# Kernel tuning notes

Hardware: AMD Instinct MI355X
Metric: run time of the kernel (lower is better)

## Reference

```python
import jax, jax.numpy as jnp
import numpy as np

MARGIN = 0.1
LAMBDA_EFFECT = 0.5

B, T_V, K, T_S = 32, 8192, 64, 128


def setup_inputs() -> dict:
    key = jax.random.key(0)
    k1, k2, k3, k4, k5 = jax.random.split(key, 5)
    pred_orig = jax.random.normal(k1, (B, T_V), dtype=jnp.float32)
    pred_intervened = jax.random.normal(k2, (K, B, T_V), dtype=jnp.float32)
    intervened_indices = jax.random.randint(k3, (K,), 0, T_S, dtype=jnp.int32)
    # GT alignment mask: sparse-ish binary alignment between frames and sentences
    gt_mask = jax.random.bernoulli(k4, 0.2, (B, T_V, T_S)).astype(jnp.int32)
    # prefix-valid video mask: valid length per batch in [T_V//2, T_V]
    lengths = jax.random.randint(k5, (B,), T_V // 2, T_V + 1, dtype=jnp.int32)
    mask_video = (jnp.arange(T_V, dtype=jnp.int32)[None, :] < lengths[:, None]).astype(jnp.int32)
    return {
        "pred_orig": pred_orig,
        "pred_intervened": pred_intervened,
        "intervened_indices": intervened_indices,
        "gt_mask": gt_mask,
        "mask_video": mask_video,
    }


def reference(pred_orig, pred_intervened, intervened_indices, gt_mask, mask_video):
    # pred_orig: [B,T], pred_intervened: [K,B,T], gt_mask: [B,T,S], mask_video: [B,T]
    prob_orig = jax.nn.sigmoid(pred_orig)                 # [B,T]
    prob_int = jax.nn.sigmoid(pred_intervened)            # [K,B,T]
    effect = jnp.abs(prob_orig[None, :, :] - prob_int)    # [K,B,T]

    valid = mask_video.astype(bool)                       # [B,T] (prefix mask == :T_v_valid slice)
    # gather intervened sentence columns: [B,T,K] -> [K,B,T]
    gt_sel = jnp.transpose(gt_mask[:, :, intervened_indices], (2, 0, 1))

    aligned = (gt_sel > 0) & valid[None]                  # [K,B,T]
    non_aligned = (gt_sel == 0) & valid[None]             # [K,B,T]

    cnt_a = aligned.sum(axis=-1)                          # [K,B]
    cnt_n = non_aligned.sum(axis=-1)                      # [K,B]

    ea = jnp.sum(effect * aligned, axis=-1) / jnp.maximum(cnt_a, 1)
    en = jnp.sum(effect * non_aligned, axis=-1) / jnp.maximum(cnt_n, 1)

    per_pair = jnp.where((cnt_a > 0) & (cnt_n > 0),
                         jax.nn.relu(MARGIN - (ea - en)),
                         jnp.zeros_like(ea))
    num_interventions = pred_orig.shape[0] * pred_intervened.shape[0]
    alignment_consistency = per_pair.sum() / max(num_interventions, 1)
    total_intervention_loss = alignment_consistency * LAMBDA_EFFECT
    return alignment_consistency, total_intervention_loss
```

## Files before the change

### kernel.cpp

```cpp
#include <hip/hip_runtime.h>
#include <cstdint>

#define BB 32
#define TV 8192
#define KK 64
#define TS 128
#define MARGIN_F 0.1f
#define LAMBDA_F 0.5f

#define TT 256
static constexpr int KSTR = BB * TV;
static constexpr int NTILE = TV / TT;


__global__ __launch_bounds__(256, 4) void fused_kernel(
    const float* __restrict__ po, const float* __restrict__ pi,
    const int* __restrict__ idx, const int* __restrict__ gt,
    const int* __restrict__ mv,
    float* __restrict__ gsa, float* __restrict__ gsv,
    float* __restrict__ gca, int* __restrict__ len) {
  const int tid = threadIdx.x;
  const int lane = tid & 63;
  const int w = tid >> 6;
  const int tile = blockIdx.x & (NTILE - 1);
  const int b = blockIdx.x >> 5;
  const int t0 = tile * TT;

  __shared__ unsigned long long planes[4][65];
  __shared__ unsigned long long sVg[4];
  __shared__ float so[TT];
  __shared__ float saL[KK][65];
  __shared__ float svL[KK][65];

  const int r0 = b * TV + t0 + w * 64;
  const unsigned long long V = __ballot(mv[r0 + lane] != 0);
  if (lane == 0) {
    sVg[w] = V;
    if (V) atomicAdd(&len[b], __popcll(V));
  }
  so[tid] = __fdividef(1.f, 1.f + __expf(-po[b * TV + t0 + tid]));

  const int c = idx[lane];
  const int csel = c & 3, csh = c >> 2;
  unsigned long long plane = 0ull;
  if (V != 0ull) {
    const int4* rowp = (const int4*)(gt + (size_t)r0 * TS);
#pragma unroll 4
    for (int ch = 0; ch < 32; ++ch) {
      int4 v = rowp[ch * 64 + lane];
      unsigned long long b0 = __ballot(v.x > 0);
      unsigned long long b1 = __ballot(v.y > 0);
      unsigned long long b2 = __ballot(v.z > 0);
      unsigned long long b3 = __ballot(v.w > 0);
      unsigned long long sel =
          (csel == 0) ? b0 : (csel == 1) ? b1 : (csel == 2) ? b2 : b3;
      const unsigned long long raw0 = (sel >> csh) & 1ull;
      const unsigned long long raw1 = (sel >> (32 + csh)) & 1ull;
      plane |= (raw0 << (2 * ch)) | (raw1 << (2 * ch + 1));
    }
    plane &= V;
  }
  planes[w][lane] = plane;
  __syncthreads();

  if ((sVg[0] | sVg[1] | sVg[2] | sVg[3]) == 0ull) return;

  const int g = lane >> 4;
  const int sh4 = (lane & 15) * 4;
  const unsigned vb4 = (unsigned)((sVg[g] >> sh4) & 15ull);
  const float4 so4 = *(const float4*)&so[lane * 4];
  const float* pib = pi + (size_t)b * TV + t0 + lane * 4;

#pragma unroll 4
  for (int kk = 0; kk < 16; ++kk) {
    const int k = w * 16 + kk;
    const float4 xi = *(const float4*)(pib + (size_t)k * KSTR);
    const unsigned ab4 = (unsigned)((planes[g][k] >> sh4) & 15ull);
    float sa = 0.f, sv = 0.f;
    {
      const float e = fabsf(so4.x - __fdividef(1.f, 1.f + __expf(-xi.x)));
      if (ab4 & 1u) sa += e;
      if (vb4 & 1u) sv += e;
    }
    {
      const float e = fabsf(so4.y - __fdividef(1.f, 1.f + __expf(-xi.y)));
      if (ab4 & 2u) sa += e;
      if (vb4 & 2u) sv += e;
    }
    {
      const float e = fabsf(so4.z - __fdividef(1.f, 1.f + __expf(-xi.z)));
      if (ab4 & 4u) sa += e;
      if (vb4 & 4u) sv += e;
    }
    {
      const float e = fabsf(so4.w - __fdividef(1.f, 1.f + __expf(-xi.w)));
      if (ab4 & 8u) sa += e;
      if (vb4 & 8u) sv += e;
    }
    saL[k][lane] = sa;
    svL[k][lane] = sv;
  }
  __syncthreads();

  if (tid < KK) {
    const int k = tid;
    float S = 0.f;
    int ca = 0;
#pragma unroll 8
    for (int j = 0; j < 64; ++j) S += saL[k][j];
#pragma unroll
    for (int gg = 0; gg < 4; ++gg) ca += __popcll(planes[gg][k]);
    atomicAdd(&gsa[k * BB + b], S);
    if (ca) atomicAdd(&gca[k * BB + b], (float)ca);
  } else if (tid < 2 * KK) {
    const int k = tid - KK;
    float S = 0.f;
#pragma unroll 8
    for (int j = 0; j < 64; ++j) S += svL[k][j];
    atomicAdd(&gsv[k * BB + b], S);
  }
}

__global__ __launch_bounds__(256) void fin_kernel(
    const float* __restrict__ gsa, const float* __restrict__ gsv,
    const float* __restrict__ gca, const int* __restrict__ len,
    float* __restrict__ out) {
  float s = 0.f;
  for (int i = threadIdx.x; i < KK * BB; i += 256) {
    const int b = i & (BB - 1);
    const float ca = gca[i];
    const float cn = (float)len[b] - ca;
    if (ca > 0.f && cn > 0.f) {
      const float sa = gsa[i];
      const float sv = gsv[i];
      const float d = MARGIN_F - (sa / ca - (sv - sa) / cn);
      s += d > 0.f ? d : 0.f;
    }
  }
#pragma unroll
  for (int off = 32; off > 0; off >>= 1) s += __shfl_down(s, off);
  __shared__ float ws4[4];
  if ((threadIdx.x & 63) == 0) ws4[threadIdx.x >> 6] = s;
  __syncthreads();
  if (threadIdx.x == 0) {
    const float S = ws4[0] + ws4[1] + ws4[2] + ws4[3];
    const float ac = S * (1.0f / (float)(KK * BB));
    out[0] = ac;
    out[1] = ac * LAMBDA_F;
  }
}

extern "C" void kernel_launch(void* const* d_in, const int* in_sizes, int n_in,
                              void* d_out, int out_size, void* d_ws, size_t ws_size,
                              hipStream_t stream) {
  const float* pred_orig = (const float*)d_in[0];
  const float* pred_int  = (const float*)d_in[1];
  const int*   idx       = (const int*)d_in[2];
  const int*   gt        = (const int*)d_in[3];
  const int*   mv        = (const int*)d_in[4];
  float* out = (float*)d_out;

  float* gsa = (float*)d_ws;
  float* gsv = gsa + KK * BB;
  float* gca = gsv + KK * BB;
  int*   len = (int*)(gca + KK * BB);

  hipMemsetAsync(d_ws, 0, (size_t)(3 * KK * BB) * sizeof(float) + BB * sizeof(int),
                 stream);
  fused_kernel<<<BB * NTILE, 256, 0, stream>>>(
      pred_orig, pred_int, idx, gt, mv, gsa, gsv, gca, len);
  fin_kernel<<<1, 256, 0, stream>>>(gsa, gsv, gca, len, out);
}
```

Measured before the change: 264.4 us.

## Halve tile size, batch gt loads, and reduce via shuffles instead of LDS

Shrinks the time tile from 256 to 128 frames, which doubles the block count, and swizzles the tile index per batch row. The gt_mask scan now issues eight int4 loads per batch before the ballots, to raise memory-level parallelism. Per-k partial sums are reduced with wavefront xor-shuffles in place of the shared-memory transpose and the second barrier. pred_intervened loads for fully invalid frame pairs are skipped. More blocks and more atomics per output element add contention and launch cost.

```diff
diff --git a/kernel.cpp b/kernel.cpp
--- a/kernel.cpp
+++ b/kernel.cpp
@@ -8,10 +8,9 @@
 #define MARGIN_F 0.1f
 #define LAMBDA_F 0.5f
 
-#define TT 256
+#define TT 128
 static constexpr int KSTR = BB * TV;
 static constexpr int NTILE = TV / TT;
-
 
 __global__ __launch_bounds__(256, 4) void fused_kernel(
     const float* __restrict__ po, const float* __restrict__ pi,
@@ -22,102 +21,108 @@
   const int tid = threadIdx.x;
   const int lane = tid & 63;
   const int w = tid >> 6;
-  const int tile = blockIdx.x & (NTILE - 1);
-  const int b = blockIdx.x >> 5;
+
+  const int bid = blockIdx.x;
+  const int b = bid >> 6;
+  const int tile = (bid & 63) ^ b;
   const int t0 = tile * TT;
 
-  __shared__ unsigned long long planes[4][65];
-  __shared__ unsigned long long sVg[4];
+  __shared__ unsigned long long ph[4][65];
+  __shared__ unsigned sV[4];
   __shared__ float so[TT];
-  __shared__ float saL[KK][65];
-  __shared__ float svL[KK][65];
 
-  const int r0 = b * TV + t0 + w * 64;
-  const unsigned long long V = __ballot(mv[r0 + lane] != 0);
+  const int rbase = b * TV + t0 + 32 * w;
+  const int mvv = (lane < 32) ? mv[rbase + lane] : 0;
+  const unsigned V32 = (unsigned)__ballot(mvv != 0);
   if (lane == 0) {
-    sVg[w] = V;
-    if (V) atomicAdd(&len[b], __popcll(V));
+    sV[w] = V32;
+    if (V32) atomicAdd(&len[b], __popc(V32));
   }
-  so[tid] = __fdividef(1.f, 1.f + __expf(-po[b * TV + t0 + tid]));
+  if (tid < TT) so[tid] = __fdividef(1.f, 1.f + __expf(-po[b * TV + t0 + tid]));
 
   const int c = idx[lane];
   const int csel = c & 3, csh = c >> 2;
+  const int h32 = (w & 1) * 32;
   unsigned long long plane = 0ull;
-  if (V != 0ull) {
-    const int4* rowp = (const int4*)(gt + (size_t)r0 * TS);
-#pragma unroll 4
-    for (int ch = 0; ch < 32; ++ch) {
-      int4 v = rowp[ch * 64 + lane];
-      unsigned long long b0 = __ballot(v.x > 0);
-      unsigned long long b1 = __ballot(v.y > 0);
-      unsigned long long b2 = __ballot(v.z > 0);
-      unsigned long long b3 = __ballot(v.w > 0);
-      unsigned long long sel =
-          (csel == 0) ? b0 : (csel == 1) ? b1 : (csel == 2) ? b2 : b3;
-      const unsigned long long raw0 = (sel >> csh) & 1ull;
-      const unsigned long long raw1 = (sel >> (32 + csh)) & 1ull;
-      plane |= (raw0 << (2 * ch)) | (raw1 << (2 * ch + 1));
+  if (V32 != 0u) {
+    const int4* rowp = (const int4*)(gt + (size_t)rbase * TS);
+#pragma unroll
+    for (int batch = 0; batch < 2; ++batch) {
+      int4 v[8];
+#pragma unroll
+      for (int i = 0; i < 8; ++i) v[i] = rowp[(batch * 8 + i) * 64 + lane];
+#pragma unroll
+      for (int i = 0; i < 8; ++i) {
+        const int it = batch * 8 + i;
+        const unsigned long long b0 = __ballot(v[i].x > 0);
+        const unsigned long long b1 = __ballot(v[i].y > 0);
+        const unsigned long long b2 = __ballot(v[i].z > 0);
+        const unsigned long long b3 = __ballot(v[i].w > 0);
+        const unsigned long long sel =
+            (csel == 0) ? b0 : (csel == 1) ? b1 : (csel == 2) ? b2 : b3;
+        plane |= ((sel >> csh) & 1ull) << (h32 + 2 * it);
+        plane |= ((sel >> (32 + csh)) & 1ull) << (h32 + 2 * it + 1);
+      }
     }
-    plane &= V;
+    plane &= ((unsigned long long)V32) << h32;
   }
-  planes[w][lane] = plane;
+  ph[w][lane] = plane;
   __syncthreads();
 
-  if ((sVg[0] | sVg[1] | sVg[2] | sVg[3]) == 0ull) return;
+  if ((sV[0] | sV[1] | sV[2] | sV[3]) == 0u) return;
 
-  const int g = lane >> 4;
-  const int sh4 = (lane & 15) * 4;
-  const unsigned vb4 = (unsigned)((sVg[g] >> sh4) & 15ull);
-  const float4 so4 = *(const float4*)&so[lane * 4];
-  const float* pib = pi + (size_t)b * TV + t0 + lane * 4;
+  const int bitpos = (lane & 31) * 2;
+  const unsigned long long Vlo =
+      (unsigned long long)sV[0] | ((unsigned long long)sV[1] << 32);
+  const unsigned long long Vhi =
+      (unsigned long long)sV[2] | ((unsigned long long)sV[3] << 32);
+  const unsigned long long myV = (lane < 32) ? Vlo : Vhi;
+  const unsigned vb2 = (unsigned)((myV >> bitpos) & 3ull);
+  const float2 so2 = *(const float2*)&so[2 * lane];
+  const float* pib = pi + (size_t)b * TV + t0 + 2 * lane;
+  const int kbase = w * 16;
 
-#pragma unroll 4
-  for (int kk = 0; kk < 16; ++kk) {
-    const int k = w * 16 + kk;
-    const float4 xi = *(const float4*)(pib + (size_t)k * KSTR);
-    const unsigned ab4 = (unsigned)((planes[g][k] >> sh4) & 15ull);
-    float sa = 0.f, sv = 0.f;
-    {
-      const float e = fabsf(so4.x - __fdividef(1.f, 1.f + __expf(-xi.x)));
-      if (ab4 & 1u) sa += e;
-      if (vb4 & 1u) sv += e;
+  float2 x[16];
+#pragma unroll
+  for (int i = 0; i < 16; ++i) {
+    x[i] = make_float2(0.f, 0.f);
+    if (vb2) x[i] = *(const float2*)(pib + (size_t)(kbase + i) * KSTR);
+  }
+
+  float sa[16], sv[16];
+#pragma unroll
+  for (int i = 0; i < 16; ++i) {
+    const int k = kbase + i;
+    const unsigned long long mine =
+        (lane < 32) ? (ph[0][k] | ph[1][k]) : (ph[2][k] | ph[3][k]);
+    const unsigned ab2 = (unsigned)((mine >> bitpos) & 3ull);
+    const float e0 = fabsf(so2.x - __fdividef(1.f, 1.f + __expf(-x[i].x)));
+    const float e1 = fabsf(so2.y - __fdividef(1.f, 1.f + __expf(-x[i].y)));
+    float a = 0.f, vv = 0.f;
+    if (vb2 & 1u) vv += e0;
+    if (vb2 & 2u) vv += e1;
+    if (ab2 & 1u) a += e0;
+    if (ab2 & 2u) a += e1;
+    sa[i] = a;
+    sv[i] = vv;
+  }
+
+#pragma unroll
+  for (int i = 0; i < 16; ++i) {
+    float A = sa[i], Vv = sv[i];
+#pragma unroll
+    for (int off = 32; off; off >>= 1) {
+      A += __shfl_xor(A, off);
+      Vv += __shfl_xor(Vv, off);
     }
-    {
-      const float e = fabsf(so4.y - __fdividef(1.f, 1.f + __expf(-xi.y)));
-      if (ab4 & 2u) sa += e;
-      if (vb4 & 2u) sv += e;
+    if (lane == 0) {
+      const int k = kbase + i;
+      if (A != 0.f) atomicAdd(&gsa[k * BB + b], A);
+      if (Vv != 0.f) atomicAdd(&gsv[k * BB + b], Vv);
+      const int ca =
+          __popcll(ph[0][k] | ph[1][k]) + __popcll(ph[2][k] | ph[3][k]);
+      if (ca) atomicAdd(&gca[k * BB + b], (float)ca);
     }
-    {
-      const float e = fabsf(so4.z - __fdividef(1.f, 1.f + __expf(-xi.z)));
-      if (ab4 & 4u) sa += e;
-      if (vb4 & 4u) sv += e;
-    }
-    {
-      const float e = fabsf(so4.w - __fdividef(1.f, 1.f + __expf(-xi.w)));
-      if (ab4 & 8u) sa += e;
-      if (vb4 & 8u) sv += e;
-    }
-    saL[k][lane] = sa;
-    svL[k][lane] = sv;
-  }
-  __syncthreads();
-
-  if (tid < KK) {
-    const int k = tid;
-    float S = 0.f;
-    int ca = 0;
-#pragma unroll 8
-    for (int j = 0; j < 64; ++j) S += saL[k][j];
-#pragma unroll
-    for (int gg = 0; gg < 4; ++gg) ca += __popcll(planes[gg][k]);
-    atomicAdd(&gsa[k * BB + b], S);
-    if (ca) atomicAdd(&gca[k * BB + b], (float)ca);
-  } else if (tid < 2 * KK) {
-    const int k = tid - KK;
-    float S = 0.f;
-#pragma unroll 8
-    for (int j = 0; j < 64; ++j) S += svL[k][j];
-    atomicAdd(&gsv[k * BB + b], S);
   }
 }
 
```

After: 303.0 us. 14.6% more time.

## Use 512-thread blocks with 32-row slices per wave and swizzle tile order

Applied to the files above, without the earlier changes.

Doubles the block to 8 waves. Each wave now handles 32 frames of the gt mask instead of 64, which halves the per-wave gather loop, and handles 8 interventions instead of 16. Bitplanes shrink to 32-bit words. Tile order is rotated per batch so that concurrently running blocks touch different memory regions. The cost is that half of each wave's lanes are idle during the mask load, plus more occupancy pressure from the larger block and the 8-blocks-per-CU launch bound.

```diff
diff --git a/kernel.cpp b/kernel.cpp
--- a/kernel.cpp
+++ b/kernel.cpp
@@ -12,8 +12,7 @@
 static constexpr int KSTR = BB * TV;
 static constexpr int NTILE = TV / TT;
 
-
-__global__ __launch_bounds__(256, 4) void fused_kernel(
+__global__ __launch_bounds__(512, 8) void fused_kernel(
     const float* __restrict__ po, const float* __restrict__ pi,
     const int* __restrict__ idx, const int* __restrict__ gt,
     const int* __restrict__ mv,
@@ -22,83 +21,79 @@
   const int tid = threadIdx.x;
   const int lane = tid & 63;
   const int w = tid >> 6;
-  const int tile = blockIdx.x & (NTILE - 1);
-  const int b = blockIdx.x >> 5;
+
+  const int bid = blockIdx.x;
+  const int b = bid >> 5;
+  const int tile = ((bid & 31) + b) & 31;
   const int t0 = tile * TT;
 
-  __shared__ unsigned long long planes[4][65];
-  __shared__ unsigned long long sVg[4];
+  __shared__ unsigned ph[8][65];
+  __shared__ unsigned sV[8];
   __shared__ float so[TT];
   __shared__ float saL[KK][65];
   __shared__ float svL[KK][65];
 
-  const int r0 = b * TV + t0 + w * 64;
-  const unsigned long long V = __ballot(mv[r0 + lane] != 0);
+  const int grow = b * TV + t0 + 32 * w;
+  const int mvv = (lane < 32) ? mv[grow + lane] : 0;
+  const unsigned V32 = (unsigned)__ballot(mvv != 0);
   if (lane == 0) {
-    sVg[w] = V;
-    if (V) atomicAdd(&len[b], __popcll(V));
+    sV[w] = V32;
+    if (V32) atomicAdd(&len[b], __popc(V32));
   }
-  so[tid] = __fdividef(1.f, 1.f + __expf(-po[b * TV + t0 + tid]));
+  if (tid < TT) so[tid] = __fdividef(1.f, 1.f + __expf(-po[b * TV + t0 + tid]));
 
   const int c = idx[lane];
   const int csel = c & 3, csh = c >> 2;
-  unsigned long long plane = 0ull;
-  if (V != 0ull) {
-    const int4* rowp = (const int4*)(gt + (size_t)r0 * TS);
+  unsigned plane = 0u;
+  if (V32 != 0u) {
+    const int4* rowp = (const int4*)(gt + (size_t)grow * TS);
 #pragma unroll 4
-    for (int ch = 0; ch < 32; ++ch) {
-      int4 v = rowp[ch * 64 + lane];
-      unsigned long long b0 = __ballot(v.x > 0);
-      unsigned long long b1 = __ballot(v.y > 0);
-      unsigned long long b2 = __ballot(v.z > 0);
-      unsigned long long b3 = __ballot(v.w > 0);
-      unsigned long long sel =
+    for (int ch = 0; ch < 16; ++ch) {
+      const int4 v = rowp[ch * 64 + lane];
+      const unsigned long long b0 = __ballot(v.x > 0);
+      const unsigned long long b1 = __ballot(v.y > 0);
+      const unsigned long long b2 = __ballot(v.z > 0);
+      const unsigned long long b3 = __ballot(v.w > 0);
+      const unsigned long long sel =
           (csel == 0) ? b0 : (csel == 1) ? b1 : (csel == 2) ? b2 : b3;
-      const unsigned long long raw0 = (sel >> csh) & 1ull;
-      const unsigned long long raw1 = (sel >> (32 + csh)) & 1ull;
-      plane |= (raw0 << (2 * ch)) | (raw1 << (2 * ch + 1));
+      plane |= (unsigned)((sel >> csh) & 1ull) << (2 * ch);
+      plane |= (unsigned)((sel >> (32 + csh)) & 1ull) << (2 * ch + 1);
     }
-    plane &= V;
+    plane &= V32;
   }
-  planes[w][lane] = plane;
+  ph[w][lane] = plane;
   __syncthreads();
 
-  if ((sVg[0] | sVg[1] | sVg[2] | sVg[3]) == 0ull) return;
+  if ((sV[0] | sV[1] | sV[2] | sV[3] | sV[4] | sV[5] | sV[6] | sV[7]) == 0u)
+    return;
 
-  const int g = lane >> 4;
-  const int sh4 = (lane & 15) * 4;
-  const unsigned vb4 = (unsigned)((sVg[g] >> sh4) & 15ull);
+  const int g2 = lane >> 3;
+  const int sh = (lane & 7) * 4;
+  const unsigned vb4 = (sV[g2] >> sh) & 15u;
   const float4 so4 = *(const float4*)&so[lane * 4];
   const float* pib = pi + (size_t)b * TV + t0 + lane * 4;
+  const int kbase = w * 8;
 
 #pragma unroll 4
-  for (int kk = 0; kk < 16; ++kk) {
-    const int k = w * 16 + kk;
-    const float4 xi = *(const float4*)(pib + (size_t)k * KSTR);
-    const unsigned ab4 = (unsigned)((planes[g][k] >> sh4) & 15ull);
-    float sa = 0.f, sv = 0.f;
-    {
-      const float e = fabsf(so4.x - __fdividef(1.f, 1.f + __expf(-xi.x)));
-      if (ab4 & 1u) sa += e;
-      if (vb4 & 1u) sv += e;
-    }
-    {
-      const float e = fabsf(so4.y - __fdividef(1.f, 1.f + __expf(-xi.y)));
-      if (ab4 & 2u) sa += e;
-      if (vb4 & 2u) sv += e;
-    }
-    {
-      const float e = fabsf(so4.z - __fdividef(1.f, 1.f + __expf(-xi.z)));
-      if (ab4 & 4u) sa += e;
-      if (vb4 & 4u) sv += e;
-    }
-    {
-      const float e = fabsf(so4.w - __fdividef(1.f, 1.f + __expf(-xi.w)));
-      if (ab4 & 8u) sa += e;
-      if (vb4 & 8u) sv += e;
-    }
-    saL[k][lane] = sa;
-    svL[k][lane] = sv;
+  for (int i = 0; i < 8; ++i) {
+    const int k = kbase + i;
+    const float4 x = *(const float4*)(pib + (size_t)k * KSTR);
+    const unsigned ab4 = (ph[g2][k] >> sh) & 15u;
+    const float e0 = fabsf(so4.x - __fdividef(1.f, 1.f + __expf(-x.x)));
+    const float e1 = fabsf(so4.y - __fdividef(1.f, 1.f + __expf(-x.y)));
+    const float e2 = fabsf(so4.z - __fdividef(1.f, 1.f + __expf(-x.z)));
+    const float e3 = fabsf(so4.w - __fdividef(1.f, 1.f + __expf(-x.w)));
+    float a = 0.f, vv = 0.f;
+    if (ab4 & 1u) a += e0;
+    if (vb4 & 1u) vv += e0;
+    if (ab4 & 2u) a += e1;
+    if (vb4 & 2u) vv += e1;
+    if (ab4 & 4u) a += e2;
+    if (vb4 & 4u) vv += e2;
+    if (ab4 & 8u) a += e3;
+    if (vb4 & 8u) vv += e3;
+    saL[k][lane] = a;
+    svL[k][lane] = vv;
   }
   __syncthreads();
 
@@ -109,7 +104,7 @@
 #pragma unroll 8
     for (int j = 0; j < 64; ++j) S += saL[k][j];
 #pragma unroll
-    for (int gg = 0; gg < 4; ++gg) ca += __popcll(planes[gg][k]);
+    for (int gg = 0; gg < 8; ++gg) ca += __popc(ph[gg][k]);
     atomicAdd(&gsa[k * BB + b], S);
     if (ca) atomicAdd(&gca[k * BB + b], (float)ca);
   } else if (tid < 2 * KK) {
@@ -167,7 +162,7 @@
 
   hipMemsetAsync(d_ws, 0, (size_t)(3 * KK * BB) * sizeof(float) + BB * sizeof(int),
                  stream);
-  fused_kernel<<<BB * NTILE, 256, 0, stream>>>(
+  fused_kernel<<<BB * NTILE, 512, 0, stream>>>(
       pred_orig, pred_int, idx, gt, mv, gsa, gsv, gca, len);
   fin_kernel<<<1, 256, 0, stream>>>(gsa, gsv, gca, len, out);
 }
```

New measurement: 289.2 us. 1.09x slower.
